# Kernel tuning notes

Hardware: AMD Instinct MI355X
Metric: run time of the kernel (lower is better)

The kernel has to match this reference:

```python
import jax, jax.numpy as jnp
import numpy as np

EPS = 1e-5  # torch InstanceNorm2d default eps


def _attend(x_q, x_kv, Wq, Wk, Wv, Wo):
    # x_q, x_kv: [B, N, C]
    B, N, _ = x_q.shape
    q = x_q @ Wq            # [B, N, CH]
    k = x_kv @ Wk           # [B, N, CH]
    v = x_kv @ Wv           # [B, N, CH]
    CH = q.shape[-1]
    # rearrange 'b n c -> n (b c)' : [N, B*CH]; the torch repeat across batch
    # is redundant (same K/V for every query sample), so we keep one copy.
    kcat = jnp.transpose(k, (1, 0, 2)).reshape(N, B * CH)
    vcat = jnp.transpose(v, (1, 0, 2)).reshape(N, B * CH)
    # scores[b, i, j] = sum_n q[b, n, i] * kcat[n, j]  -> [B, CH, B*CH]
    scores = jnp.einsum('bni,nj->bij', q, kcat)
    # InstanceNorm2d(1): per-sample normalization over the (CH, B*CH) plane
    mu = scores.mean(axis=(1, 2), keepdims=True)
    var = scores.var(axis=(1, 2), keepdims=True)  # biased var, matches torch
    scores = (scores - mu) * jax.lax.rsqrt(var + EPS)
    attn = jax.nn.softmax(scores, axis=-1)        # softmax over j (dim=3)
    # ctx[b, n, i] = sum_j attn[b, i, j] * vcat[n, j]  -> [B, N, CH]
    ctx = jnp.einsum('bij,nj->bni', attn, vcat)
    return ctx @ Wo  # [B, N, C]


def setup_inputs() -> dict:
    key = jax.random.key(0)
    k0, k1, k2, k3, k4 = jax.random.split(key, 5)
    C, H = 64, 8
    CH = C * H
    emb = jax.random.normal(k0, (16, 2048, C), dtype=jnp.float32)
    s = 0.02
    Wq = jax.random.normal(k1, (C, CH), dtype=jnp.float32) * s
    Wk = jax.random.normal(k2, (C, CH), dtype=jnp.float32) * s
    Wv = jax.random.normal(k3, (C, CH), dtype=jnp.float32) * s
    Wo = jax.random.normal(k4, (CH, C), dtype=jnp.float32) * s
    return {"emb": emb, "Wq": Wq, "Wk": Wk, "Wv": Wv, "Wo": Wo}


def reference(emb, Wq, Wk, Wv, Wo):
    emb_l, emb_u = jnp.split(emb, 2, axis=0)
    emb_u_sg = jax.lax.stop_gradient(emb_u)  # emb_u is detached in the torch code
    out_u2l = _attend(emb_u_sg, emb_l, Wq, Wk, Wv, Wo)
    out_l2u = _attend(emb_l, emb_u_sg, Wq, Wk, Wv, Wo)
    return jnp.concatenate([out_l2u, out_u2l], axis=0)
```

## Files before the change

### kernel.cpp

```cpp
#include <hip/hip_runtime.h>
#include <hip/hip_fp16.h>

#define EPS 1e-5f

typedef __attribute__((ext_vector_type(8))) _Float16 half8;
typedef __attribute__((ext_vector_type(4))) float float4v;

template<int BM, int BN, int BK, int TM, int TN, typename TA, typename TC>
__global__ __launch_bounds__((BM/TM)*(BN/TN))
void gemm_tn(const TA* __restrict__ A, const float* __restrict__ B,
             TC* __restrict__ C, int K,
             int lda, int ldb, int ldc,
             int divA, long long bsAd, int modA, long long bsAm,
             int divB, long long bsBd, int modB, long long bsBm,
             int divC, long long bsCd, int modC, long long bsCm)
{
    constexpr int T  = (BM/TM)*(BN/TN);
    constexpr int HM = TM/2, HN = TN/2;
    __shared__ float As[BK][BM];
    __shared__ float Bs[BK][BN];

    const int tid = threadIdx.x;
    const int z = blockIdx.z;
    const int n0 = blockIdx.x * BN;
    const int m0 = blockIdx.y * BM;
    A += (long long)(z / divA) * bsAd + (long long)(z % modA) * bsAm;
    B += (long long)(z / divB) * bsBd + (long long)(z % modB) * bsBm;
    C += (long long)(z / divC) * bsCd + (long long)(z % modC) * bsCm;

    const int tx = tid % (BN/TN);
    const int ty = tid / (BN/TN);

    float acc[TM][TN] = {};

    for (int k0 = 0; k0 < K; k0 += BK) {
#pragma unroll
        for (int idx = tid * 4; idx < BK * BM; idx += T * 4) {
            int rr = idx / BM, cc = idx % BM;
            *(float4*)&As[rr][cc] = *(const float4*)(A + (long long)(k0 + rr) * lda + m0 + cc);
        }
#pragma unroll
        for (int idx = tid * 4; idx < BK * BN; idx += T * 4) {
            int rr = idx / BN, cc = idx % BN;
            *(float4*)&Bs[rr][cc] = *(const float4*)(B + (long long)(k0 + rr) * ldb + n0 + cc);
        }
        __syncthreads();
#pragma unroll
        for (int kk = 0; kk < BK; kk++) {
            float a[TM], b[TN];
#pragma unroll
            for (int u = 0; u < HM; u++) {
                a[u]      = As[kk][ty * HM + u];
                a[HM + u] = As[kk][BM / 2 + ty * HM + u];
            }
#pragma unroll
            for (int v = 0; v < HN; v++) {
                b[v]      = Bs[kk][tx * HN + v];
                b[HN + v] = Bs[kk][BN / 2 + tx * HN + v];
            }
#pragma unroll
            for (int u = 0; u < TM; u++)
#pragma unroll
                for (int v = 0; v < TN; v++)
                    acc[u][v] += a[u] * b[v];
        }
        __syncthreads();
    }

#pragma unroll
    for (int u = 0; u < TM; u++) {
        int rl = (u < HM) ? ty * HM + u : BM / 2 + ty * HM + (u - HM);
        TC* cr = C + (long long)(m0 + rl) * ldc + n0;
        if constexpr (sizeof(TC) == 2) {
#pragma unroll
            for (int v = 0; v < HN; v++) {
                cr[tx * HN + v]          = __float2half(acc[u][v]);
                cr[BN / 2 + tx * HN + v] = __float2half(acc[u][HN + v]);
            }
        } else {
#pragma unroll
            for (int v = 0; v < HN; v++) {
                cr[tx * HN + v] = acc[u][v];
                cr[BN / 2 + tx * HN + v] = acc[u][HN + v];
            }
        }
    }
}

__device__ __forceinline__ float rv_from(const float* sums2, int db)
{
    float s1 = 0.f, s2 = 0.f;
#pragma unroll
    for (int p = 0; p < 8; p++) {
        s1 += sums2[(db * 8 + p) * 2];
        s2 += sums2[(db * 8 + p) * 2 + 1];
    }
    const float inv = 1.f / 2097152.f;
    float mu = s1 * inv;
    float var = s2 * inv - mu * mu;
    return rsqrtf(var + EPS);
}

__global__ __launch_bounds__(256)
void prep_k(const float* __restrict__ emb, const float* __restrict__ Wq,
            const float* __restrict__ Wk, const float* __restrict__ Wv,
            const float* __restrict__ Wo, float* __restrict__ Gpart,
            __half* __restrict__ WkT16, __half* __restrict__ Wo16,
            __half* __restrict__ Wv16, float* __restrict__ GWQpart,
            float* __restrict__ wsp)
{
    __shared__ __align__(16) char smem[18432];
    const int tid = threadIdx.x;
    const int bid = blockIdx.x;

    if (bid < 512) {
        __half (*As)[72] = (__half(*)[72])smem;
        __half (*Bs)[72] = (__half(*)[72])(smem + 9216);
        const int ks = bid >> 6;
        const int z6 = bid & 63;
        const int b  = z6 >> 3;
        const int bp = z6 & 7;
        const float* Xq  = emb + (long long)b * 131072;
        const float* Xkv = emb + 1048576 + (long long)bp * 131072;

        const int lane = tid & 63, w = tid >> 6, q = lane >> 4, l16 = lane & 15;
        const int tok = tid & 63;
        const int cg  = w * 16;

        float4v acc[4];
#pragma unroll
        for (int nt = 0; nt < 4; nt++) acc[nt] = (float4v)0.f;

        for (int t0 = ks * 256; t0 < ks * 256 + 256; t0 += 64) {
            const float* q4 = Xq  + (long long)(t0 + tok) * 64 + cg;
            const float* k4 = Xkv + (long long)(t0 + tok) * 64 + cg;
#pragma unroll
            for (int j = 0; j < 4; j++) {
                float4 v = *(const float4*)(q4 + j * 4);
                As[cg + j * 4 + 0][tok] = __float2half(v.x);
                As[cg + j * 4 + 1][tok] = __float2half(v.y);
                As[cg + j * 4 + 2][tok] = __float2half(v.z);
                As[cg + j * 4 + 3][tok] = __float2half(v.w);
                float4 u = *(const float4*)(k4 + j * 4);
                Bs[cg + j * 4 + 0][tok] = __float2half(u.x);
                Bs[cg + j * 4 + 1][tok] = __float2half(u.y);
                Bs[cg + j * 4 + 2][tok] = __float2half(u.z);
                Bs[cg + j * 4 + 3][tok] = __float2half(u.w);
            }
            __syncthreads();
#pragma unroll
            for (int kc = 0; kc < 64; kc += 32) {
                half8 af = *(const half8*)&As[w * 16 + l16][kc + q * 8];
                half8 bf[4];
#pragma unroll
                for (int nt = 0; nt < 4; nt++)
                    bf[nt] = *(const half8*)&Bs[nt * 16 + l16][kc + q * 8];
#pragma unroll
                for (int nt = 0; nt < 4; nt++)
                    acc[nt] = __builtin_amdgcn_mfma_f32_16x16x32_f16(af, bf[nt], acc[nt], 0, 0, 0);
            }
            __syncthreads();
        }

        float* Gz = Gpart + (long long)ks * 262144 + (long long)z6 * 4096;
#pragma unroll
        for (int nt = 0; nt < 4; nt++)
#pragma unroll
            for (int t = 0; t < 4; t++) {
                int m = w * 16 + q * 4 + t;
                Gz[m * 64 + nt * 16 + l16] = acc[nt][t];
            }
    } else if (bid < 528) {
        float (*t)[65] = (float(*)[65])smem;
        const int which = (bid - 512) >> 3;
        const int c0 = ((bid - 512) & 7) * 64;
        const int c = tid & 63, r4 = tid >> 6;
        if (which == 0) {
#pragma unroll
            for (int rr = r4; rr < 64; rr += 4)
                t[rr][c] = Wk[rr * 512 + c0 + c];
            __syncthreads();
#pragma unroll
            for (int rr = r4; rr < 64; rr += 4)
                WkT16[(c0 + rr) * 64 + c] = __float2half(t[c][rr]);
        } else {
#pragma unroll
            for (int rr = r4; rr < 64; rr += 4)
                t[rr][c] = Wo[(c0 + rr) * 64 + c];
            __syncthreads();
#pragma unroll
            for (int rr = r4; rr < 64; rr += 4)
                Wo16[rr * 512 + c0 + c] = __float2half(t[c][rr]);
        }
    } else if (bid < 536) {
        const int base = (bid - 528) * 4096;
#pragma unroll
        for (int it = 0; it < 4; it++) {
            int e = base + (tid + it * 256) * 4;
            float4 v = *(const float4*)(Wv + e);
            *(__half2*)(Wv16 + e)     = __floats2half2_rn(v.x, v.y);
            *(__half2*)(Wv16 + e + 2) = __floats2half2_rn(v.z, v.w);
        }
    } else {
        float (*Wl)[68] = (float(*)[68])smem;
        const int t2 = bid - 536;
        const int which = t2 >> 3;
        const int sl = t2 & 7;
        const int i0 = sl * 64;
        const float* W = which ? Wq : Wk;
        float* Gout = GWQpart + (long long)(which * 8 + sl) * 4096;
#pragma unroll
        for (int it = 0; it < 4; it++) {
            int e = tid + it * 256;
            int cc = e >> 4, i4 = (e & 15) * 4;
            *(float4*)&Wl[cc][i4] = *(const float4*)(W + cc * 512 + i0 + i4);
        }
        __syncthreads();
        if (tid < 64) {
            float s = 0.f;
#pragma unroll
            for (int j = 0; j < 64; j++) s += Wl[tid][j];
            wsp[(which * 8 + sl) * 64 + tid] = s;
        }
        const int cr = tid >> 2, cg = (tid & 3) * 16;
        float p[16] = {};
        for (int k = 0; k < 64; k++) {
            float a = Wl[cr][k];
#pragma unroll
            for (int j = 0; j < 16; j++) p[j] += a * Wl[cg + j][k];
        }
#pragma unroll
        for (int j = 0; j < 16; j++)
            Gout[cr * 64 + cg + j] = p[j];
    }
}

__global__ __launch_bounds__(256)
void stats2_k(const float* __restrict__ Gpart, const float* __restrict__ GWQpart,
              const float* __restrict__ wsp, float* __restrict__ Gred,
              float* __restrict__ sums2)
{
    __shared__ float Graw[64][68], Gs[64][68], GQs[64][68], GWs[64][68];
    __shared__ float wqsS[64], wksS[64];
    const int tid = threadIdx.x;
    const int z = blockIdx.x;
    const int d = z >> 6, b = (z >> 3) & 7, bp = z & 7;
    const int zm = d ? (bp * 8 + b) : (b * 8 + bp);

    for (int f = tid * 4; f < 4096; f += 1024) {
        float4 g = make_float4(0.f, 0.f, 0.f, 0.f);
        float4 gw = g, gq = g;
#pragma unroll
        for (int s = 0; s < 8; s++) {
            float4 p = *(const float4*)(Gpart + (long long)s * 262144 + (long long)zm * 4096 + f);
            g.x += p.x; g.y += p.y; g.z += p.z; g.w += p.w;
            float4 w1 = *(const float4*)(GWQpart + (long long)s * 4096 + f);
            gw.x += w1.x; gw.y += w1.y; gw.z += w1.z; gw.w += w1.w;
            float4 q1 = *(const float4*)(GWQpart + (long long)(8 + s) * 4096 + f);
            gq.x += q1.x; gq.y += q1.y; gq.z += q1.z; gq.w += q1.w;
        }
        int rr = f >> 6, cc = f & 63;
        *(float4*)&Graw[rr][cc] = g;
        *(float4*)&GWs[rr][cc] = gw;
        *(float4*)&GQs[rr][cc] = gq;
    }
    if (tid < 64) {
        float a = 0.f, bsum = 0.f;
#pragma unroll
        for (int s = 0; s < 8; s++) {
            bsum += wsp[s * 64 + tid];
            a    += wsp[(8 + s) * 64 + tid];
        }
        wqsS[tid] = a; wksS[tid] = bsum;
    }
    __syncthreads();
    for (int e = tid; e < 4096; e += 256) {
        int rr = e >> 6, cc = e & 63;
        Gs[rr][cc] = d ? Graw[cc][rr] : Graw[rr][cc];
    }
    __syncthreads();
    for (int f = tid * 4; f < 4096; f += 1024)
        *(float4*)(Gred + (long long)z * 4096 + f) = *(float4*)&Gs[f >> 6][f & 63];

    const int r = tid >> 2;
    const int c0 = (tid & 3) * 16;
    float p1[16] = {}, p2[16] = {};
    for (int k = 0; k < 64; k++) {
        float gq = GQs[r][k], g = Gs[r][k];
#pragma unroll
        for (int j = 0; j < 16; j++) {
            p1[j] += gq * Gs[k][c0 + j];
            p2[j] += g  * GWs[k][c0 + j];
        }
    }
    float s2 = 0.f;
#pragma unroll
    for (int j = 0; j < 16; j++) s2 += p1[j] * p2[j];
    float s1 = 0.f;
    const float wq = wqsS[r];
#pragma unroll
    for (int j = 0; j < 16; j++) s1 += wq * Gs[r][c0 + j] * wksS[c0 + j];

    const int lane = tid & 63, w = tid >> 6;
#pragma unroll
    for (int off = 32; off; off >>= 1) {
        s1 += __shfl_down(s1, off, 64);
        s2 += __shfl_down(s2, off, 64);
    }
    __shared__ float r1[4], r2[4];
    if (lane == 0) { r1[w] = s1; r2[w] = s2; }
    __syncthreads();
    if (tid == 0) {
        sums2[z * 2]     = r1[0] + r1[1] + r1[2] + r1[3];
        sums2[z * 2 + 1] = r2[0] + r2[1] + r2[2] + r2[3];
    }
}

__global__ __launch_bounds__(256)
void mfma_ms(const __half* __restrict__ E16, const __half* __restrict__ WkT16,
             const __half* __restrict__ Wv16, const float* __restrict__ sums2,
             float* __restrict__ rsp, __half* __restrict__ Mt)
{
    __shared__ __half Es[128][72];
    __shared__ __half Wks[64][72];
    __shared__ __half Wvs[64][72];
    __shared__ __half Pt[128][72];

    const int tid = threadIdx.x;
    const int z = blockIdx.x;
    const int it = blockIdx.y;
    const int db = z >> 3, bp = z & 7;
    const int i0base = it * 128;
    const __half* Ez = E16 + (long long)z * 32768 + (long long)i0base * 64;

#pragma unroll
    for (int k = 0; k < 4; k++) {
        int e = tid + k * 256;
        int row = e >> 3, c8 = (e & 7) * 8;
        *(half8*)&Es[row][c8] = *(const half8*)(Ez + row * 64 + c8);
    }

    const int lane = tid & 63, w = tid >> 6, q = lane >> 4, l16 = lane & 15;
    const float rv = rv_from(sums2, db);

    float4v macc[2][4];
#pragma unroll
    for (int a = 0; a < 2; a++)
#pragma unroll
        for (int b2 = 0; b2 < 4; b2++) macc[a][b2] = (float4v)0.f;
    float rsacc[2] = {0.f, 0.f};

    const int srow = tid >> 2, sc8 = (tid & 3) * 16;

    for (int ch0 = 0; ch0 < 512; ch0 += 64) {
        __syncthreads();
        *(half8*)&Wks[srow][sc8]     = *(const half8*)(WkT16 + (long long)(ch0 + srow) * 64 + sc8);
        *(half8*)&Wks[srow][sc8 + 8] = *(const half8*)(WkT16 + (long long)(ch0 + srow) * 64 + sc8 + 8);
        *(half8*)&Wvs[srow][sc8]     = *(const half8*)(Wv16 + (long long)srow * 512 + ch0 + sc8);
        *(half8*)&Wvs[srow][sc8 + 8] = *(const half8*)(Wv16 + (long long)srow * 512 + ch0 + sc8 + 8);
        __syncthreads();

        float4v sacc[4][2];
#pragma unroll
        for (int a = 0; a < 4; a++)
#pragma unroll
            for (int b2 = 0; b2 < 2; b2++) sacc[a][b2] = (float4v)0.f;
#pragma unroll
        for (int kc = 0; kc < 64; kc += 32) {
            half8 af[4], bf[2];
#pragma unroll
            for (int mt = 0; mt < 4; mt++)
                af[mt] = *(const half8*)&Wks[mt * 16 + l16][kc + q * 8];
#pragma unroll
            for (int nt = 0; nt < 2; nt++)
                bf[nt] = *(const half8*)&Es[w * 32 + nt * 16 + l16][kc + q * 8];
#pragma unroll
            for (int mt = 0; mt < 4; mt++)
#pragma unroll
                for (int nt = 0; nt < 2; nt++)
                    sacc[mt][nt] = __builtin_amdgcn_mfma_f32_16x16x32_f16(af[mt], bf[nt], sacc[mt][nt], 0, 0, 0);
        }

#pragma unroll
        for (int nt = 0; nt < 2; nt++) {
            const int i = w * 32 + nt * 16 + l16;
#pragma unroll
            for (int mt = 0; mt < 4; mt++) {
                float e0 = __expf(rv * sacc[mt][nt][0]);
                float e1 = __expf(rv * sacc[mt][nt][1]);
                float e2 = __expf(rv * sacc[mt][nt][2]);
                float e3 = __expf(rv * sacc[mt][nt][3]);
                rsacc[nt] += e0 + e1 + e2 + e3;
                const int ch = mt * 16 + q * 4;
                *(__half2*)&Pt[i][ch]     = __floats2half2_rn(e0, e1);
                *(__half2*)&Pt[i][ch + 2] = __floats2half2_rn(e2, e3);
            }
        }
        __syncthreads();

#pragma unroll
        for (int kc = 0; kc < 64; kc += 32) {
            half8 af2[2], bf2[4];
#pragma unroll
            for (int mt2 = 0; mt2 < 2; mt2++)
                af2[mt2] = *(const half8*)&Pt[w * 32 + mt2 * 16 + l16][kc + q * 8];
#pragma unroll
            for (int nt2 = 0; nt2 < 4; nt2++)
                bf2[nt2] = *(const half8*)&Wvs[nt2 * 16 + l16][kc + q * 8];
#pragma unroll
            for (int mt2 = 0; mt2 < 2; mt2++)
#pragma unroll
                for (int nt2 = 0; nt2 < 4; nt2++)
                    macc[mt2][nt2] = __builtin_amdgcn_mfma_f32_16x16x32_f16(af2[mt2], bf2[nt2], macc[mt2][nt2], 0, 0, 0);
        }
    }

#pragma unroll
    for (int nt = 0; nt < 2; nt++) {
        float p = rsacc[nt];
        p += __shfl_xor(p, 16, 64);
        p += __shfl_xor(p, 32, 64);
        if (q == 0)
            rsp[(long long)(db * 512 + i0base + w * 32 + nt * 16 + l16) * 8 + bp] = p;
    }
    __syncthreads();

    __half (*MtS)[144] = (__half(*)[144])&Pt[0][0];
    const float sc = 1.f / 4096.f;
#pragma unroll
    for (int mt2 = 0; mt2 < 2; mt2++)
#pragma unroll
        for (int nt2 = 0; nt2 < 4; nt2++) {
            const int cp = nt2 * 16 + l16;
            const int il = w * 32 + mt2 * 16 + q * 4;
#pragma unroll
            for (int t = 0; t < 4; t++)
                MtS[cp][il + t] = __float2half(macc[mt2][nt2][t] * sc);
        }
    __syncthreads();
    __half* Mz = Mt + (long long)z * 32768;
    {
        const int row = tid >> 2, seg = (tid & 3) * 32;
#pragma unroll
        for (int j = 0; j < 4; j++)
            *(half8*)(Mz + (long long)row * 512 + i0base + seg + j * 8) =
                *(const half8*)&MtS[row][seg + j * 8];
    }
}

__global__ __launch_bounds__(256)
void mfma_n(const __half* __restrict__ Mt, const __half* __restrict__ Wo16,
            const float* __restrict__ rsp, __half* __restrict__ NT)
{
    __shared__ __half Mts[64][72];
    __shared__ __half Wos[64][72];
    __shared__ float invrS[64];
    const int tid = threadIdx.x;
    const int db = blockIdx.x >> 3, bp = blockIdx.x & 7;
    const __half* Mz = Mt + (long long)(db * 8 + bp) * 32768;
    const int lane = tid & 63, w = tid >> 6, q = lane >> 4, l16 = lane & 15;

    float4v acc[4];
#pragma unroll
    for (int mt = 0; mt < 4; mt++) acc[mt] = (float4v)0.f;

    const int srow = tid >> 2, sc8 = (tid & 3) * 16;

    for (int i0 = 0; i0 < 512; i0 += 64) {
        __syncthreads();
        if (tid < 64) {
            const float* rp = rsp + (long long)(db * 512 + i0 + tid) * 8;
            float4 a = *(const float4*)rp;
            float4 b = *(const float4*)(rp + 4);
            invrS[tid] = 4096.0f / (a.x + a.y + a.z + a.w + b.x + b.y + b.z + b.w);
        }
        __syncthreads();
#pragma unroll
        for (int h = 0; h < 2; h++) {
            half8 v = *(const half8*)(Mz + (long long)srow * 512 + i0 + sc8 + h * 8);
            half8 o;
#pragma unroll
            for (int j = 0; j < 8; j++)
                o[j] = (_Float16)((float)v[j] * invrS[sc8 + h * 8 + j]);
            *(half8*)&Mts[srow][sc8 + h * 8] = o;
            *(half8*)&Wos[srow][sc8 + h * 8] =
                *(const half8*)(Wo16 + (long long)srow * 512 + i0 + sc8 + h * 8);
        }
        __syncthreads();
#pragma unroll
        for (int kc = 0; kc < 64; kc += 32) {
            half8 af[4];
#pragma unroll
            for (int mt = 0; mt < 4; mt++)
                af[mt] = *(const half8*)&Mts[mt * 16 + l16][kc + q * 8];
            half8 bf = *(const half8*)&Wos[w * 16 + l16][kc + q * 8];
#pragma unroll
            for (int mt = 0; mt < 4; mt++)
                acc[mt] = __builtin_amdgcn_mfma_f32_16x16x32_f16(af[mt], bf, acc[mt], 0, 0, 0);
        }
    }

    __half* Nz = NT + (long long)db * 32768;
    const int o = w * 16 + l16;
#pragma unroll
    for (int mt = 0; mt < 4; mt++) {
        const int k = bp * 64 + mt * 16 + q * 4;
        *(__half2*)(Nz + (long long)o * 512 + k)     = __floats2half2_rn(acc[mt][0], acc[mt][1]);
        *(__half2*)(Nz + (long long)o * 512 + k + 2) = __floats2half2_rn(acc[mt][2], acc[mt][3]);
    }
}

__global__ __launch_bounds__(256)
void mfma_out(const float* __restrict__ emb, const __half* __restrict__ NT,
              float* __restrict__ out)
{
    __shared__ __half Xs[128][72];
    __shared__ __half Bs[64][72];
    const int tid = threadIdx.x;
    const int db = blockIdx.y;
    const int d = db >> 3;
    const int n0 = blockIdx.x * 128;
    const float* Xb = emb + (long long)(1 - d) * 1048576;
    const __half* Bz = NT + (long long)db * 32768;

    const int lane = tid & 63, w = tid >> 6, q = lane >> 4, l16 = lane & 15;

    float4v acc[2][4];
#pragma unroll
    for (int a = 0; a < 2; a++)
#pragma unroll
        for (int b = 0; b < 4; b++) acc[a][b] = (float4v)0.f;

    for (int bp = 0; bp < 8; bp++) {
        const float* src = Xb + (long long)bp * 131072 + (long long)n0 * 64;
#pragma unroll
        for (int it = 0; it < 8; it++) {
            int e = (tid + it * 256) * 4;
            int row = e >> 6, col = e & 63;
            float4 v = *(const float4*)(src + (long long)row * 64 + col);
            *(__half2*)&Xs[row][col]     = __floats2half2_rn(v.x, v.y);
            *(__half2*)&Xs[row][col + 2] = __floats2half2_rn(v.z, v.w);
        }
        {
            int o = tid >> 2, c8 = (tid & 3) * 16;
            *(half8*)&Bs[o][c8]     = *(const half8*)(Bz + o * 512 + bp * 64 + c8);
            *(half8*)&Bs[o][c8 + 8] = *(const half8*)(Bz + o * 512 + bp * 64 + c8 + 8);
        }
        __syncthreads();
#pragma unroll
        for (int kc = 0; kc < 64; kc += 32) {
            half8 af[2], bf[4];
#pragma unroll
            for (int mt = 0; mt < 2; mt++)
                af[mt] = *(const half8*)&Xs[w * 32 + mt * 16 + l16][kc + q * 8];
#pragma unroll
            for (int ot = 0; ot < 4; ot++)
                bf[ot] = *(const half8*)&Bs[ot * 16 + l16][kc + q * 8];
#pragma unroll
            for (int mt = 0; mt < 2; mt++)
#pragma unroll
                for (int ot = 0; ot < 4; ot++)
                    acc[mt][ot] = __builtin_amdgcn_mfma_f32_16x16x32_f16(af[mt], bf[ot], acc[mt][ot], 0, 0, 0);
        }
        __syncthreads();
    }

    float* Od = out + (long long)db * 131072;
#pragma unroll
    for (int mt = 0; mt < 2; mt++)
#pragma unroll
        for (int ot = 0; ot < 4; ot++)
#pragma unroll
            for (int t = 0; t < 4; t++) {
                int n = n0 + w * 32 + mt * 16 + q * 4 + t;
                Od[(long long)n * 64 + ot * 16 + l16] = acc[mt][ot][t];
            }
}

extern "C" void kernel_launch(void* const* d_in, const int* in_sizes, int n_in,
                              void* d_out, int out_size, void* d_ws, size_t ws_size,
                              hipStream_t stream)
{
    const float* emb = (const float*)d_in[0];
    const float* Wq  = (const float*)d_in[1];
    const float* Wk  = (const float*)d_in[2];
    const float* Wv  = (const float*)d_in[3];
    const float* Wo  = (const float*)d_in[4];
    float* out = (float*)d_out;
    float* ws  = (float*)d_ws;

    float* Gpart   = ws;
    float* GWQpart = ws + 2097152;
    float* wsp     = ws + 2162688;
    float* sums2   = ws + 2163712;
    float* Gred    = ws + 2163968;
    float* rsp     = ws + 2688256;
    __half* E16    = (__half*)(ws + 2753792);
    __half* WkT16  = (__half*)(ws + 4850944);
    __half* Wv16   = (__half*)(ws + 4867328);
    __half* Wo16   = (__half*)(ws + 4883712);
    __half* Mt     = (__half*)(ws + 4900096);
    __half* NT     = (__half*)(ws + 6997248);

    prep_k<<<552, 256, 0, stream>>>(emb, Wq, Wk, Wv, Wo, Gpart, WkT16, Wo16,
                                    Wv16, GWQpart, wsp);

    stats2_k<<<128, 256, 0, stream>>>(Gpart, GWQpart, wsp, Gred, sums2);

    gemm_tn<64, 64, 16, 4, 4, float, __half><<<dim3(1, 8, 128), 256, 0, stream>>>(
        Wq, Gred, E16, 64, 512, 64, 64,
        1, 0LL, 1, 0LL,
        1, 4096LL, 1, 0LL,
        1, 32768LL, 1, 0LL);

    mfma_ms<<<dim3(128, 4), 256, 0, stream>>>(E16, WkT16, Wv16, sums2, rsp, Mt);

    mfma_n<<<128, 256, 0, stream>>>(Mt, Wo16, rsp, NT);

    mfma_out<<<dim3(16, 16), 256, 0, stream>>>(emb, NT, out);
}
```

Baseline: 167.0 us.

## Fuse Wq·G projection into mfma_ms using split-fp16 MFMA

Removes the separate fp32 SIMT gemm_tn launch that produced E16 = Wq^T·G and computes that product inside mfma_ms instead. It uses a hi/lo fp16 split (three MFMAs per tile) to keep near-fp32 accuracy. prep_k gains blocks that transpose Wq into hi/lo fp16 buffers, and stats2_k now writes G transposed as hi/lo fp16 rather than fp32. This saves one kernel launch and the E16 round trip through global memory. In exchange, every mfma_ms block recomputes its E tile with extra MFMA work and reads global memory directly with no LDS staging.

```diff
diff --git a/kernel.cpp b/kernel.cpp
--- a/kernel.cpp
+++ b/kernel.cpp
@@ -5,87 +5,6 @@
 
 typedef __attribute__((ext_vector_type(8))) _Float16 half8;
 typedef __attribute__((ext_vector_type(4))) float float4v;
-
-template<int BM, int BN, int BK, int TM, int TN, typename TA, typename TC>
-__global__ __launch_bounds__((BM/TM)*(BN/TN))
-void gemm_tn(const TA* __restrict__ A, const float* __restrict__ B,
-             TC* __restrict__ C, int K,
-             int lda, int ldb, int ldc,
-             int divA, long long bsAd, int modA, long long bsAm,
-             int divB, long long bsBd, int modB, long long bsBm,
-             int divC, long long bsCd, int modC, long long bsCm)
-{
-    constexpr int T  = (BM/TM)*(BN/TN);
-    constexpr int HM = TM/2, HN = TN/2;
-    __shared__ float As[BK][BM];
-    __shared__ float Bs[BK][BN];
-
-    const int tid = threadIdx.x;
-    const int z = blockIdx.z;
-    const int n0 = blockIdx.x * BN;
-    const int m0 = blockIdx.y * BM;
-    A += (long long)(z / divA) * bsAd + (long long)(z % modA) * bsAm;
-    B += (long long)(z / divB) * bsBd + (long long)(z % modB) * bsBm;
-    C += (long long)(z / divC) * bsCd + (long long)(z % modC) * bsCm;
-
-    const int tx = tid % (BN/TN);
-    const int ty = tid / (BN/TN);
-
-    float acc[TM][TN] = {};
-
-    for (int k0 = 0; k0 < K; k0 += BK) {
-#pragma unroll
-        for (int idx = tid * 4; idx < BK * BM; idx += T * 4) {
-            int rr = idx / BM, cc = idx % BM;
-            *(float4*)&As[rr][cc] = *(const float4*)(A + (long long)(k0 + rr) * lda + m0 + cc);
-        }
-#pragma unroll
-        for (int idx = tid * 4; idx < BK * BN; idx += T * 4) {
-            int rr = idx / BN, cc = idx % BN;
-            *(float4*)&Bs[rr][cc] = *(const float4*)(B + (long long)(k0 + rr) * ldb + n0 + cc);
-        }
-        __syncthreads();
-#pragma unroll
-        for (int kk = 0; kk < BK; kk++) {
-            float a[TM], b[TN];
-#pragma unroll
-            for (int u = 0; u < HM; u++) {
-                a[u]      = As[kk][ty * HM + u];
-                a[HM + u] = As[kk][BM / 2 + ty * HM + u];
-            }
-#pragma unroll
-            for (int v = 0; v < HN; v++) {
-                b[v]      = Bs[kk][tx * HN + v];
-                b[HN + v] = Bs[kk][BN / 2 + tx * HN + v];
-            }
-#pragma unroll
-            for (int u = 0; u < TM; u++)
-#pragma unroll
-                for (int v = 0; v < TN; v++)
-                    acc[u][v] += a[u] * b[v];
-        }
-        __syncthreads();
-    }
-
-#pragma unroll
-    for (int u = 0; u < TM; u++) {
-        int rl = (u < HM) ? ty * HM + u : BM / 2 + ty * HM + (u - HM);
-        TC* cr = C + (long long)(m0 + rl) * ldc + n0;
-        if constexpr (sizeof(TC) == 2) {
-#pragma unroll
-            for (int v = 0; v < HN; v++) {
-                cr[tx * HN + v]          = __float2half(acc[u][v]);
-                cr[BN / 2 + tx * HN + v] = __float2half(acc[u][HN + v]);
-            }
-        } else {
-#pragma unroll
-            for (int v = 0; v < HN; v++) {
-                cr[tx * HN + v] = acc[u][v];
-                cr[BN / 2 + tx * HN + v] = acc[u][HN + v];
-            }
-        }
-    }
-}
 
 __device__ __forceinline__ float rv_from(const float* sums2, int db)
 {
@@ -107,7 +26,8 @@
             const float* __restrict__ Wo, float* __restrict__ Gpart,
             __half* __restrict__ WkT16, __half* __restrict__ Wo16,
             __half* __restrict__ Wv16, float* __restrict__ GWQpart,
-            float* __restrict__ wsp)
+            float* __restrict__ wsp, __half* __restrict__ WqT16h,
+            __half* __restrict__ WqT16l)
 {
     __shared__ __align__(16) char smem[18432];
     const int tid = threadIdx.x;
@@ -201,7 +121,7 @@
             *(__half2*)(Wv16 + e)     = __floats2half2_rn(v.x, v.y);
             *(__half2*)(Wv16 + e + 2) = __floats2half2_rn(v.z, v.w);
         }
-    } else {
+    } else if (bid < 552) {
         float (*Wl)[68] = (float(*)[68])smem;
         const int t2 = bid - 536;
         const int which = t2 >> 3;
@@ -232,13 +152,28 @@
 #pragma unroll
         for (int j = 0; j < 16; j++)
             Gout[cr * 64 + cg + j] = p[j];
+    } else {
+        float (*t)[65] = (float(*)[65])smem;
+        const int i0 = (bid - 552) * 64;
+        const int c = tid & 63, r4 = tid >> 6;
+#pragma unroll
+        for (int rr = r4; rr < 64; rr += 4)
+            t[rr][c] = Wq[rr * 512 + i0 + c];
+        __syncthreads();
+#pragma unroll
+        for (int rr = r4; rr < 64; rr += 4) {
+            float x = t[c][rr];
+            __half h = __float2half(x);
+            WqT16h[(i0 + rr) * 64 + c] = h;
+            WqT16l[(i0 + rr) * 64 + c] = __float2half(x - __half2float(h));
+        }
     }
 }
 
 __global__ __launch_bounds__(256)
 void stats2_k(const float* __restrict__ Gpart, const float* __restrict__ GWQpart,
-              const float* __restrict__ wsp, float* __restrict__ Gred,
-              float* __restrict__ sums2)
+              const float* __restrict__ wsp, __half* __restrict__ GT16h,
+              __half* __restrict__ GT16l, float* __restrict__ sums2)
 {
     __shared__ float Graw[64][68], Gs[64][68], GQs[64][68], GWs[64][68];
     __shared__ float wqsS[64], wksS[64];
@@ -279,8 +214,13 @@
         Gs[rr][cc] = d ? Graw[cc][rr] : Graw[rr][cc];
     }
     __syncthreads();
-    for (int f = tid * 4; f < 4096; f += 1024)
-        *(float4*)(Gred + (long long)z * 4096 + f) = *(float4*)&Gs[f >> 6][f & 63];
+    for (int e = tid; e < 4096; e += 256) {
+        int cp = e >> 6, c = e & 63;
+        float g = Gs[c][cp];
+        __half h = __float2half(g);
+        GT16h[(long long)z * 4096 + e] = h;
+        GT16l[(long long)z * 4096 + e] = __float2half(g - __half2float(h));
+    }
 
     const int r = tid >> 2;
     const int c0 = (tid & 3) * 16;
@@ -317,9 +257,11 @@
 }
 
 __global__ __launch_bounds__(256)
-void mfma_ms(const __half* __restrict__ E16, const __half* __restrict__ WkT16,
-             const __half* __restrict__ Wv16, const float* __restrict__ sums2,
-             float* __restrict__ rsp, __half* __restrict__ Mt)
+void mfma_ms(const __half* __restrict__ WqT16h, const __half* __restrict__ WqT16l,
+             const __half* __restrict__ GT16h, const __half* __restrict__ GT16l,
+             const __half* __restrict__ WkT16, const __half* __restrict__ Wv16,
+             const float* __restrict__ sums2, float* __restrict__ rsp,
+             __half* __restrict__ Mt)
 {
     __shared__ __half Es[128][72];
     __shared__ __half Wks[64][72];
@@ -331,17 +273,53 @@
     const int it = blockIdx.y;
     const int db = z >> 3, bp = z & 7;
     const int i0base = it * 128;
-    const __half* Ez = E16 + (long long)z * 32768 + (long long)i0base * 64;
-
-#pragma unroll
-    for (int k = 0; k < 4; k++) {
-        int e = tid + k * 256;
-        int row = e >> 3, c8 = (e & 7) * 8;
-        *(half8*)&Es[row][c8] = *(const half8*)(Ez + row * 64 + c8);
-    }
 
     const int lane = tid & 63, w = tid >> 6, q = lane >> 4, l16 = lane & 15;
     const float rv = rv_from(sums2, db);
+
+    {
+        const __half* Wh = WqT16h + (long long)i0base * 64;
+        const __half* Wl = WqT16l + (long long)i0base * 64;
+        const __half* Gh = GT16h + (long long)z * 4096;
+        const __half* Gl = GT16l + (long long)z * 4096;
+        float4v eacc[2][4];
+#pragma unroll
+        for (int a = 0; a < 2; a++)
+#pragma unroll
+            for (int b2 = 0; b2 < 4; b2++) eacc[a][b2] = (float4v)0.f;
+#pragma unroll
+        for (int kc = 0; kc < 64; kc += 32) {
+            half8 ah[2], al[2], bh[4], bl[4];
+#pragma unroll
+            for (int mt = 0; mt < 2; mt++) {
+                const int i = w * 32 + mt * 16 + l16;
+                ah[mt] = *(const half8*)(Wh + i * 64 + kc + q * 8);
+                al[mt] = *(const half8*)(Wl + i * 64 + kc + q * 8);
+            }
+#pragma unroll
+            for (int nt = 0; nt < 4; nt++) {
+                const int cp = nt * 16 + l16;
+                bh[nt] = *(const half8*)(Gh + cp * 64 + kc + q * 8);
+                bl[nt] = *(const half8*)(Gl + cp * 64 + kc + q * 8);
+            }
+#pragma unroll
+            for (int mt = 0; mt < 2; mt++)
+#pragma unroll
+                for (int nt = 0; nt < 4; nt++) {
+                    eacc[mt][nt] = __builtin_amdgcn_mfma_f32_16x16x32_f16(ah[mt], bh[nt], eacc[mt][nt], 0, 0, 0);
+                    eacc[mt][nt] = __builtin_amdgcn_mfma_f32_16x16x32_f16(ah[mt], bl[nt], eacc[mt][nt], 0, 0, 0);
+                    eacc[mt][nt] = __builtin_amdgcn_mfma_f32_16x16x32_f16(al[mt], bh[nt], eacc[mt][nt], 0, 0, 0);
+                }
+        }
+#pragma unroll
+        for (int mt = 0; mt < 2; mt++)
+#pragma unroll
+            for (int nt = 0; nt < 4; nt++)
+#pragma unroll
+                for (int t = 0; t < 4; t++)
+                    Es[w * 32 + mt * 16 + q * 4 + t][nt * 16 + l16] =
+                        __float2half(eacc[mt][nt][t]);
+    }
 
     float4v macc[2][4];
 #pragma unroll
@@ -593,27 +571,24 @@
     float* GWQpart = ws + 2097152;
     float* wsp     = ws + 2162688;
     float* sums2   = ws + 2163712;
-    float* Gred    = ws + 2163968;
+    __half* GT16h  = (__half*)(ws + 2163968);
+    __half* GT16l  = (__half*)(ws + 2426112);
     float* rsp     = ws + 2688256;
-    __half* E16    = (__half*)(ws + 2753792);
-    __half* WkT16  = (__half*)(ws + 4850944);
-    __half* Wv16   = (__half*)(ws + 4867328);
-    __half* Wo16   = (__half*)(ws + 4883712);
-    __half* Mt     = (__half*)(ws + 4900096);
-    __half* NT     = (__half*)(ws + 6997248);
-
-    prep_k<<<552, 256, 0, stream>>>(emb, Wq, Wk, Wv, Wo, Gpart, WkT16, Wo16,
-                                    Wv16, GWQpart, wsp);
-
-    stats2_k<<<128, 256, 0, stream>>>(Gpart, GWQpart, wsp, Gred, sums2);
-
-    gemm_tn<64, 64, 16, 4, 4, float, __half><<<dim3(1, 8, 128), 256, 0, stream>>>(
-        Wq, Gred, E16, 64, 512, 64, 64,
-        1, 0LL, 1, 0LL,
-        1, 4096LL, 1, 0LL,
-        1, 32768LL, 1, 0LL);
-
-    mfma_ms<<<dim3(128, 4), 256, 0, stream>>>(E16, WkT16, Wv16, sums2, rsp, Mt);
+    __half* WkT16  = (__half*)(ws + 2753792);
+    __half* Wv16   = (__half*)(ws + 2770176);
+    __half* Wo16   = (__half*)(ws + 2786560);
+    __half* WqT16h = (__half*)(ws + 2802944);
+    __half* WqT16l = (__half*)(ws + 2819328);
+    __half* Mt     = (__half*)(ws + 2835712);
+    __half* NT     = (__half*)(ws + 4932864);
+
+    prep_k<<<560, 256, 0, stream>>>(emb, Wq, Wk, Wv, Wo, Gpart, WkT16, Wo16,
+                                    Wv16, GWQpart, wsp, WqT16h, WqT16l);
+
+    stats2_k<<<128, 256, 0, stream>>>(Gpart, GWQpart, wsp, GT16h, GT16l, sums2);
+
+    mfma_ms<<<dim3(128, 4), 256, 0, stream>>>(WqT16h, WqT16l, GT16h, GT16l,
+                                              WkT16, Wv16, sums2, rsp, Mt);
 
     mfma_n<<<128, 256, 0, stream>>>(Mt, Wo16, rsp, NT);
 
```

New measurement: 159.1 us. 1.05x faster.
